# Performance work log

Hardware: AMD Instinct MI355X
Metric: run time of the kernel (lower is better)

Reference implementation:

```python
import jax, jax.numpy as jnp
import numpy as np

B, N, C, IC = 8, 4096, 1024, 256
EPS = 1e-5


def setup_inputs() -> dict:
    key = jax.random.key(0)
    ks = jax.random.split(key, 10)
    s = 0.02  # keep activations well-scaled
    return {
        "v": jax.random.normal(ks[0], (B, N, C), jnp.float32),
        "g_w": jax.random.normal(ks[1], (IC, C), jnp.float32) * s,
        "g_b": jax.random.normal(ks[2], (IC,), jnp.float32) * s,
        "theta_w": jax.random.normal(ks[3], (IC, C), jnp.float32) * s,
        "theta_b": jax.random.normal(ks[4], (IC,), jnp.float32) * s,
        "phi_w": jax.random.normal(ks[5], (IC, C), jnp.float32) * s,
        "phi_b": jax.random.normal(ks[6], (IC,), jnp.float32) * s,
        "W_w": jax.random.normal(ks[7], (C, IC), jnp.float32) * s,
        "W_b": jax.random.normal(ks[8], (C,), jnp.float32) * s,
        "bn_gamma": jnp.ones((C,), jnp.float32),
        "bn_beta": jnp.zeros((C,), jnp.float32),
    }


def reference(v, g_w, g_b, theta_w, theta_b, phi_w, phi_b, W_w, W_b, bn_gamma, bn_beta):
    # v: (B, N, C). All Conv1d(k=1) == per-token matmul.
    g_v = jnp.einsum("bnc,ic->bni", v, g_w) + g_b          # (B, N, IC)
    theta_v = jnp.einsum("bnc,ic->bni", v, theta_w) + theta_b
    phi_v = jnp.einsum("bnc,ic->bni", v, phi_w) + phi_b
    n = v.shape[1]
    # Affinity: R = theta @ phi^T, normalized by N (no softmax)
    R = jnp.einsum("bni,bmi->bnm", theta_v, phi_v) / n      # (B, N, N)
    y = jnp.einsum("bnm,bmi->bni", R, g_v)                  # (B, N, IC)
    W_y = jnp.einsum("bni,ci->bnc", y, W_w) + W_b           # (B, N, C)
    # BatchNorm1d training mode: per-channel stats over (B, N), biased var
    mean = jnp.mean(W_y, axis=(0, 1))
    var = jnp.var(W_y, axis=(0, 1))
    W_y = (W_y - mean) * jax.lax.rsqrt(var + EPS) * bn_gamma + bn_beta
    return W_y + v                                          # residual, (B, N, C)
```

## Files before the change

kernel.cpp:

```cpp
#include <hip/hip_runtime.h>
#include <hip/hip_bf16.h>
#include <stdint.h>


using bf16 = __hip_bfloat16;
typedef __attribute__((ext_vector_type(8))) short short8;
typedef __attribute__((ext_vector_type(4))) float f32x4;
typedef __attribute__((ext_vector_type(4))) short short4v;

#define DEVI static __device__ __forceinline__

DEVI float bf2f(unsigned short u) {
  union { unsigned int i; float f; } x; x.i = ((unsigned int)u) << 16; return x.f;
}
DEVI unsigned short f2bf(float f) {
  __hip_bfloat16 h = __float2bfloat16(f);
  return *reinterpret_cast<unsigned short*>(&h);
}

DEVI void gld16(const void* g, void* l) {
  __builtin_amdgcn_global_load_lds((__attribute__((address_space(1))) void*)g,
                                   (__attribute__((address_space(3))) void*)l,
                                   16, 0, 0);
}

DEVI short8 cvt8(float4 a, float4 b) {
  short8 o;
  o[0] = (short)f2bf(a.x); o[1] = (short)f2bf(a.y);
  o[2] = (short)f2bf(a.z); o[3] = (short)f2bf(a.w);
  o[4] = (short)f2bf(b.x); o[5] = (short)f2bf(b.y);
  o[6] = (short)f2bf(b.z); o[7] = (short)f2bf(b.w);
  return o;
}

DEVI void mfma_loop(const bf16* A, int ldA, const bf16* B, int ldB,
                    int kiters, bf16* lds_a, bf16* lds_b, f32x4 acc[4][4])
{
  const int tid = threadIdx.x;
  const int lane = tid & 63;
  const int w = tid >> 6;
  const int wr = w >> 1, wc = w & 1;
  const int srow = w * 32 + (lane >> 2);
  const int scol = (((lane & 3) ^ ((srow >> 1) & 3))) * 8;
  const bf16* ga0 = A + (size_t)srow * ldA + scol;
  const bf16* ga1 = A + (size_t)(srow + 16) * ldA + scol;
  const bf16* gb0 = B + (size_t)srow * ldB + scol;
  const bf16* gb1 = B + (size_t)(srow + 16) * ldB + scol;
  bf16* la0 = lds_a + w * 1024 + lane * 8;
  bf16* la1 = la0 + 512;
  bf16* lb0 = lds_b + w * 1024 + lane * 8;
  bf16* lb1 = lb0 + 512;
  const int frow = lane & 15;
  const int fk = (((lane >> 4) ^ ((frow >> 1) & 3))) * 8;
  const bf16* ra = lds_a + (wr * 64 + frow) * 32 + fk;
  const bf16* rb = lds_b + (wc * 64 + frow) * 32 + fk;
  for (int it = 0; it < kiters; ++it) {
    gld16(ga0, la0); gld16(ga1, la1);
    gld16(gb0, lb0); gld16(gb1, lb1);
    ga0 += 32; ga1 += 32; gb0 += 32; gb1 += 32;
    __syncthreads();
    short8 af[4], bfr[4];
#pragma unroll
    for (int i = 0; i < 4; ++i) af[i] = *(const short8*)(ra + i * 512);
#pragma unroll
    for (int j = 0; j < 4; ++j) bfr[j] = *(const short8*)(rb + j * 512);
#pragma unroll
    for (int i = 0; i < 4; ++i)
#pragma unroll
      for (int j = 0; j < 4; ++j)
        acc[i][j] = __builtin_amdgcn_mfma_f32_16x16x32_bf16(af[i], bfr[j], acc[i][j], 0, 0, 0);
    __syncthreads();
  }
}

DEVI void mfma_loop64(const bf16* A, int ldA, const bf16* B, int ldB,
                      int kiters64, bf16* lds_a, bf16* lds_b, f32x4 acc[4][4])
{
  const int tid = threadIdx.x;
  const int lane = tid & 63;
  const int w = tid >> 6;
  const int wr = w >> 1, wc = w & 1;
  const bf16* gA[4]; const bf16* gB[4]; bf16* dA[4]; bf16* dB[4];
#pragma unroll
  for (int s = 0; s < 4; ++s) {
    const int p = s * 256 + tid;
    const int ksub = p >> 9;
    const int row = (p >> 2) & 127;
    const int c2 = p & 3;
    gA[s] = A + (size_t)row * ldA + ksub * 32 + c2 * 8;
    gB[s] = B + (size_t)row * ldB + ksub * 32 + c2 * 8;
    dA[s] = lds_a + s * 2048 + w * 512 + lane * 8;
    dB[s] = lds_b + s * 2048 + w * 512 + lane * 8;
  }
  const int frow = lane & 15;
  const int fk = (lane >> 4) * 8;
  const bf16* ra = lds_a + (wr * 64 + frow) * 32 + fk;
  const bf16* rb = lds_b + (wc * 64 + frow) * 32 + fk;
  for (int it = 0; it < kiters64; ++it) {
#pragma unroll
    for (int s = 0; s < 4; ++s) gld16(gA[s], dA[s]);
#pragma unroll
    for (int s = 0; s < 4; ++s) gld16(gB[s], dB[s]);
#pragma unroll
    for (int s = 0; s < 4; ++s) { gA[s] += 64; gB[s] += 64; }
    __syncthreads();
#pragma unroll
    for (int kk = 0; kk < 2; ++kk) {
      short8 af[4], bfr[4];
#pragma unroll
      for (int i = 0; i < 4; ++i) af[i] = *(const short8*)(ra + kk * 4096 + i * 512);
#pragma unroll
      for (int j = 0; j < 4; ++j) bfr[j] = *(const short8*)(rb + kk * 4096 + j * 512);
#pragma unroll
      for (int i = 0; i < 4; ++i)
#pragma unroll
        for (int j = 0; j < 4; ++j)
          acc[i][j] = __builtin_amdgcn_mfma_f32_16x16x32_bf16(af[i], bfr[j], acc[i][j], 0, 0, 0);
    }
    __syncthreads();
  }
}

#define ACC_INIT(acc)                                   \
  _Pragma("unroll") for (int i = 0; i < 4; ++i)         \
  _Pragma("unroll") for (int j = 0; j < 4; ++j)         \
      acc[i][j] = (f32x4){0.f, 0.f, 0.f, 0.f};

__global__ __launch_bounds__(256) void k_cast_all(
    const float* __restrict__ v, bf16* __restrict__ vbf,
    const float* __restrict__ s0, const float* __restrict__ s1,
    const float* __restrict__ s2, const float* __restrict__ s3,
    bf16* __restrict__ d0, bf16* __restrict__ d1,
    bf16* __restrict__ d2, bf16* __restrict__ d3,
    float* __restrict__ zbuf)
{
  const int bx = blockIdx.x;
  if (bx == 16384 + 512) {
    float4 z = {0.f, 0.f, 0.f, 0.f};
    *(float4*)(zbuf + threadIdx.x * 8) = z;
    *(float4*)(zbuf + threadIdx.x * 8 + 4) = z;
    return;
  }
  const float* in; bf16* out; size_t base;
  if (bx < 16384) {
    in = v; out = vbf; base = (size_t)bx * 2048;
  } else {
    const int wq = bx - 16384;
    switch (wq >> 7) {
      case 0:  in = s0; out = d0; break;
      case 1:  in = s1; out = d1; break;
      case 2:  in = s2; out = d2; break;
      default: in = s3; out = d3; break;
    }
    base = (size_t)(wq & 127) * 2048;
  }
  const size_t idx = base + (size_t)threadIdx.x * 8;
  float4 a = *(const float4*)(in + idx);
  float4 b = *(const float4*)(in + idx + 4);
  *(short8*)(out + idx) = cvt8(a, b);
}

__global__ __launch_bounds__(256) void k_proj(
    const bf16* __restrict__ vbf,
    const bf16* __restrict__ w_th, const float* __restrict__ b_th,
    const bf16* __restrict__ w_ph, const float* __restrict__ b_ph,
    const bf16* __restrict__ w_g,  const float* __restrict__ b_g,
    bf16* __restrict__ theta, bf16* __restrict__ phiT, bf16* __restrict__ gT)
{
  __shared__ __align__(16) char smem[34048];
  bf16* lds_a = (bf16*)smem;
  bf16* lds_b = (bf16*)(smem + 16384);
  unsigned short* lds_t = (unsigned short*)smem;

  const int tt = blockIdx.x;
  const int yy = blockIdx.y;
  const int proj = yy >> 1;
  const int icb = (yy & 1) * 128;
  const bf16* wsel = (proj == 0) ? w_th : ((proj == 1) ? w_ph : w_g);
  const float* bsel = (proj == 0) ? b_th : ((proj == 1) ? b_ph : b_g);

  const size_t t0 = (size_t)tt * 128;
  f32x4 acc[4][4];
  ACC_INIT(acc);
  mfma_loop64(vbf + t0 * 1024, 1024, wsel + (size_t)icb * 1024, 1024, 16, lds_a, lds_b, acc);

  const int tid = threadIdx.x, lane = tid & 63, w = tid >> 6;
  const int wr = w >> 1, wc = w & 1, quad = lane >> 4, l15 = lane & 15;
  float biasv[4];
#pragma unroll
  for (int j = 0; j < 4; ++j) biasv[j] = bsel[icb + wc * 64 + j * 16 + l15];

  if (proj == 0) {
#pragma unroll
    for (int i = 0; i < 4; ++i)
#pragma unroll
      for (int j = 0; j < 4; ++j)
#pragma unroll
        for (int r = 0; r < 4; ++r) {
          int m = wr * 64 + i * 16 + quad * 4 + r;
          int n = wc * 64 + j * 16 + l15;
          theta[(t0 + m) * 256 + icb + n] = __float2bfloat16(acc[i][j][r] + biasv[j]);
        }
  } else {
#pragma unroll
    for (int i = 0; i < 4; ++i)
#pragma unroll
      for (int j = 0; j < 4; ++j)
#pragma unroll
        for (int r = 0; r < 4; ++r) {
          int m = wr * 64 + i * 16 + quad * 4 + r;
          int n = wc * 64 + j * 16 + l15;
          lds_t[m * 133 + n] = f2bf(acc[i][j][r] + biasv[j]);
        }
    __syncthreads();
    bf16* outT = (proj == 1) ? phiT : gT;
    const int bb = (int)(t0 >> 12);
    const int n0 = (int)(t0 & 4095);
    const int tg = tid & 7;
    const int ch0 = tid >> 3;
#pragma unroll
    for (int half = 0; half < 2; ++half)
#pragma unroll
      for (int cc = 0; cc < 4; ++cc) {
        int ch = ch0 + cc * 32;
        int tok0 = half * 64 + tg * 8;
        short8 pk;
#pragma unroll
        for (int r = 0; r < 8; ++r) pk[r] = (short)lds_t[(tok0 + r) * 133 + ch];
        *(short8*)(outT + ((size_t)(bb * 256 + icb + ch)) * 4096 + n0 + tok0) = pk;
      }
  }
}

__global__ __launch_bounds__(256) void k_affin(
    const bf16* __restrict__ phiT, const bf16* __restrict__ gT, float* __restrict__ Mp)
{
  __shared__ __align__(16) char smem[16384];
  bf16* lds_a = (bf16*)smem;
  bf16* lds_b = (bf16*)(smem + 8192);
  const int kc = blockIdx.x;
  const int jt = blockIdx.y >> 1;
  const int it2 = blockIdx.y & 1;
  const int bb = blockIdx.z;
  f32x4 acc[4][4];
  ACC_INIT(acc);
  const bf16* A = phiT + ((size_t)bb * 256 + jt * 128) * 4096 + kc * 512;
  const bf16* B = gT   + ((size_t)bb * 256 + it2 * 128) * 4096 + kc * 512;
  mfma_loop(A, 4096, B, 4096, 16, lds_a, lds_b, acc);
  const int tid = threadIdx.x, lane = tid & 63, w = tid >> 6;
  const int wr = w >> 1, wc = w & 1, quad = lane >> 4, l15 = lane & 15;
  float* Mb = Mp + ((size_t)kc * 8 + bb) * 65536;
#pragma unroll
  for (int i = 0; i < 4; ++i)
#pragma unroll
    for (int j = 0; j < 4; ++j)
#pragma unroll
      for (int r = 0; r < 4; ++r) {
        int m = wr * 64 + i * 16 + quad * 4 + r;
        int n = wc * 64 + j * 16 + l15;
        Mb[(size_t)(jt * 128 + m) * 256 + it2 * 128 + n] = acc[i][j][r];
      }
}

__global__ __launch_bounds__(256) void k_mconv(const float* __restrict__ Mp, bf16* __restrict__ Mbf)
{
  const size_t i = ((size_t)blockIdx.x * 256 + threadIdx.x) * 4;
  float4 s = *(const float4*)(Mp + i);
#pragma unroll
  for (int kc = 1; kc < 8; ++kc) {
    float4 p = *(const float4*)(Mp + (size_t)kc * 524288 + i);
    s.x += p.x; s.y += p.y; s.z += p.z; s.w += p.w;
  }
  short4v o;
  o[0] = (short)f2bf(s.x * (1.0f / 4096.0f));
  o[1] = (short)f2bf(s.y * (1.0f / 4096.0f));
  o[2] = (short)f2bf(s.z * (1.0f / 4096.0f));
  o[3] = (short)f2bf(s.w * (1.0f / 4096.0f));
  *(short4v*)(Mbf + i) = o;
}

__global__ __launch_bounds__(256) void k_pt(
    const bf16* __restrict__ Ww, const bf16* __restrict__ Mbf, bf16* __restrict__ PT)
{
  __shared__ __align__(16) char smem[16384];
  bf16* lds_a = (bf16*)smem;
  bf16* lds_b = (bf16*)(smem + 8192);
  const int ct = blockIdx.x;
  const int jt = blockIdx.y;
  const int bb = blockIdx.z;
  f32x4 acc[4][4];
  ACC_INIT(acc);
  mfma_loop(Ww + (size_t)ct * 128 * 256, 256,
            Mbf + ((size_t)bb * 256 + jt * 128) * 256, 256, 8, lds_a, lds_b, acc);
  const int tid = threadIdx.x, lane = tid & 63, w = tid >> 6;
  const int wr = w >> 1, wc = w & 1, quad = lane >> 4, l15 = lane & 15;
#pragma unroll
  for (int i = 0; i < 4; ++i)
#pragma unroll
    for (int j = 0; j < 4; ++j)
#pragma unroll
      for (int r = 0; r < 4; ++r) {
        int m = wr * 64 + i * 16 + quad * 4 + r;
        int n = wc * 64 + j * 16 + l15;
        PT[((size_t)bb * 1024 + ct * 128 + m) * 256 + jt * 128 + n] = __float2bfloat16(acc[i][j][r]);
      }
}

__global__ __launch_bounds__(256) void k_wy(
    const bf16* __restrict__ theta, const bf16* __restrict__ PT, bf16* __restrict__ Wy,
    float* __restrict__ sums, float* __restrict__ sumsq)
{
  __shared__ __align__(16) char smem[16384];
  bf16* lds_a = (bf16*)smem;
  bf16* lds_b = (bf16*)(smem + 8192);
  const size_t t0 = (size_t)blockIdx.x * 128;
  const int ct = blockIdx.y;
  const int bb = (int)(t0 >> 12);
  f32x4 acc[4][4];
  ACC_INIT(acc);
  mfma_loop(theta + t0 * 256, 256,
            PT + ((size_t)bb * 1024 + ct * 128) * 256, 256, 8, lds_a, lds_b, acc);
  const int tid = threadIdx.x, lane = tid & 63, w = tid >> 6;
  const int wr = w >> 1, wc = w & 1, quad = lane >> 4, l15 = lane & 15;
  float ps[4] = {0.f, 0.f, 0.f, 0.f}, pq[4] = {0.f, 0.f, 0.f, 0.f};
#pragma unroll
  for (int i = 0; i < 4; ++i)
#pragma unroll
    for (int j = 0; j < 4; ++j)
#pragma unroll
      for (int r = 0; r < 4; ++r) {
        int m = wr * 64 + i * 16 + quad * 4 + r;
        int n = wc * 64 + j * 16 + l15;
        float f = acc[i][j][r];
        Wy[(t0 + m) * 1024 + ct * 128 + n] = __float2bfloat16(f);
        ps[j] += f; pq[j] += f * f;
      }
#pragma unroll
  for (int j = 0; j < 4; ++j) {
    ps[j] += __shfl_xor(ps[j], 16); ps[j] += __shfl_xor(ps[j], 32);
    pq[j] += __shfl_xor(pq[j], 16); pq[j] += __shfl_xor(pq[j], 32);
  }
  if (quad == 0) {
#pragma unroll
    for (int j = 0; j < 4; ++j) {
      int c = ct * 128 + wc * 64 + j * 16 + l15;
      atomicAdd(&sums[c], ps[j]);
      atomicAdd(&sumsq[c], pq[j]);
    }
  }
}

__global__ __launch_bounds__(256) void k_out(const bf16* __restrict__ Wy, const float* __restrict__ v,
                                             const float* __restrict__ sums, const float* __restrict__ sumsq,
                                             const float* __restrict__ gamma, const float* __restrict__ beta,
                                             float* __restrict__ out)
{
  const size_t idx = ((size_t)blockIdx.x * 256 + threadIdx.x) * 4;
  const int c = (int)(idx & 1023);
  float4 sm = *(const float4*)(sums + c);
  float4 sq = *(const float4*)(sumsq + c);
  float4 gm = *(const float4*)(gamma + c);
  float4 bt = *(const float4*)(beta + c);
  short4v wv = *(const short4v*)(Wy + idx);
  float4 vv = *(const float4*)(v + idx);
  float4 o;
#pragma unroll
  for (int k = 0; k < 4; ++k) {
    float smk = (&sm.x)[k], sqk = (&sq.x)[k], gmk = (&gm.x)[k], btk = (&bt.x)[k];
    float mean = smk * (1.0f / 32768.0f);
    float var = sqk * (1.0f / 32768.0f) - mean * mean;
    float sc = gmk * rsqrtf(var + 1e-5f);
    float sh = btk - mean * sc;
    (&o.x)[k] = bf2f((unsigned short)wv[k]) * sc + sh + (&vv.x)[k];
  }
  *(float4*)(out + idx) = o;
}

extern "C" void kernel_launch(void* const* d_in, const int* in_sizes, int n_in,
                              void* d_out, int out_size, void* d_ws, size_t ws_size,
                              hipStream_t stream)
{
  (void)in_sizes; (void)n_in; (void)out_size; (void)ws_size;
  const float* v    = (const float*)d_in[0];
  const float* g_w  = (const float*)d_in[1];
  const float* g_b  = (const float*)d_in[2];
  const float* th_w = (const float*)d_in[3];
  const float* th_b = (const float*)d_in[4];
  const float* ph_w = (const float*)d_in[5];
  const float* ph_b = (const float*)d_in[6];
  const float* W_w  = (const float*)d_in[7];
  const float* gamma = (const float*)d_in[9];
  const float* beta  = (const float*)d_in[10];
  float* out = (float*)d_out;

  char* ws = (char*)d_ws;
  bf16* vbf  = (bf16*)ws;
  bf16* Wy   = (bf16*)ws;
  float* Mp  = (float*)ws;
  ws += (size_t)32768 * 1024 * 2;
  bf16* theta = (bf16*)ws;  ws += (size_t)32768 * 256 * 2;
  bf16* phiT  = (bf16*)ws;  ws += (size_t)32768 * 256 * 2;
  bf16* gT    = (bf16*)ws;  ws += (size_t)32768 * 256 * 2;
  bf16* Mbf   = (bf16*)ws;  ws += (size_t)8 * 65536 * 2;
  bf16* PT    = (bf16*)ws;  ws += (size_t)8 * 1024 * 256 * 2;
  bf16* thwb  = (bf16*)ws;  ws += (size_t)256 * 1024 * 2;
  bf16* phwb  = (bf16*)ws;  ws += (size_t)256 * 1024 * 2;
  bf16* gwb   = (bf16*)ws;  ws += (size_t)256 * 1024 * 2;
  bf16* Wwb   = (bf16*)ws;  ws += (size_t)1024 * 256 * 2;
  float* sums = (float*)ws; ws += 4096;
  float* sumsq= (float*)ws; ws += 4096;

  k_cast_all<<<16384 + 512 + 1, 256, 0, stream>>>(v, vbf, th_w, ph_w, g_w, W_w,
                                                  thwb, phwb, gwb, Wwb, sums);

  k_proj <<<dim3(256, 6), 256, 0, stream>>>(vbf, thwb, th_b, phwb, ph_b, gwb, g_b, theta, phiT, gT);
  k_affin<<<dim3(8, 4, 8), 256, 0, stream>>>(phiT, gT, Mp);
  k_mconv<<<512, 256, 0, stream>>>(Mp, Mbf);
  k_pt   <<<dim3(8, 2, 8), 256, 0, stream>>>(Wwb, Mbf, PT);
  k_wy   <<<dim3(256, 8), 256, 0, stream>>>(theta, PT, Wy, sums, sumsq);
  k_out  <<<32768, 256, 0, stream>>>(Wy, v, sums, sumsq, gamma, beta, out);
}
```

Before: 451.0 us.

## Enlarge projection GEMM tile to 256x128 with 512-thread blocks

The projection kernel now processes 256 tokens per block using 8 waves instead of 128 tokens with 4 waves. The shared weight (B) tile is loaded once per block for twice as many rows, which halves weight traffic per token. The transposed epilogue is split into two halves that reuse the LDS staging buffer. LDS use rises to 48KB per block and there are half as many blocks, which may lower occupancy and reduce latency hiding.

```diff
diff --git a/kernel.cpp b/kernel.cpp
--- a/kernel.cpp
+++ b/kernel.cpp
@@ -73,24 +73,32 @@
   }
 }
 
-DEVI void mfma_loop64(const bf16* A, int ldA, const bf16* B, int ldB,
-                      int kiters64, bf16* lds_a, bf16* lds_b, f32x4 acc[4][4])
+DEVI void mfma_loop_256x128(const bf16* A, int ldA, const bf16* B, int ldB,
+                            int kiters64, bf16* lds_a, bf16* lds_b, f32x4 acc[4][4])
 {
   const int tid = threadIdx.x;
   const int lane = tid & 63;
   const int w = tid >> 6;
   const int wr = w >> 1, wc = w & 1;
-  const bf16* gA[4]; const bf16* gB[4]; bf16* dA[4]; bf16* dB[4];
+  const bf16* gA[4]; bf16* dA[4];
 #pragma unroll
   for (int s = 0; s < 4; ++s) {
-    const int p = s * 256 + tid;
+    const int p = s * 512 + tid;
+    const int ksub = p >> 10;
+    const int row = (p >> 2) & 255;
+    const int c2 = p & 3;
+    gA[s] = A + (size_t)row * ldA + ksub * 32 + c2 * 8;
+    dA[s] = lds_a + p * 8;
+  }
+  const bf16* gB[2]; bf16* dB[2];
+#pragma unroll
+  for (int s = 0; s < 2; ++s) {
+    const int p = s * 512 + tid;
     const int ksub = p >> 9;
     const int row = (p >> 2) & 127;
     const int c2 = p & 3;
-    gA[s] = A + (size_t)row * ldA + ksub * 32 + c2 * 8;
     gB[s] = B + (size_t)row * ldB + ksub * 32 + c2 * 8;
-    dA[s] = lds_a + s * 2048 + w * 512 + lane * 8;
-    dB[s] = lds_b + s * 2048 + w * 512 + lane * 8;
+    dB[s] = lds_b + p * 8;
   }
   const int frow = lane & 15;
   const int fk = (lane >> 4) * 8;
@@ -100,15 +108,17 @@
 #pragma unroll
     for (int s = 0; s < 4; ++s) gld16(gA[s], dA[s]);
 #pragma unroll
-    for (int s = 0; s < 4; ++s) gld16(gB[s], dB[s]);
-#pragma unroll
-    for (int s = 0; s < 4; ++s) { gA[s] += 64; gB[s] += 64; }
+    for (int s = 0; s < 2; ++s) gld16(gB[s], dB[s]);
+#pragma unroll
+    for (int s = 0; s < 4; ++s) gA[s] += 64;
+#pragma unroll
+    for (int s = 0; s < 2; ++s) gB[s] += 64;
     __syncthreads();
 #pragma unroll
     for (int kk = 0; kk < 2; ++kk) {
       short8 af[4], bfr[4];
 #pragma unroll
-      for (int i = 0; i < 4; ++i) af[i] = *(const short8*)(ra + kk * 4096 + i * 512);
+      for (int i = 0; i < 4; ++i) af[i] = *(const short8*)(ra + kk * 8192 + i * 512);
 #pragma unroll
       for (int j = 0; j < 4; ++j) bfr[j] = *(const short8*)(rb + kk * 4096 + j * 512);
 #pragma unroll
@@ -160,16 +170,16 @@
   *(short8*)(out + idx) = cvt8(a, b);
 }
 
-__global__ __launch_bounds__(256) void k_proj(
+__global__ __launch_bounds__(512) void k_proj(
     const bf16* __restrict__ vbf,
     const bf16* __restrict__ w_th, const float* __restrict__ b_th,
     const bf16* __restrict__ w_ph, const float* __restrict__ b_ph,
     const bf16* __restrict__ w_g,  const float* __restrict__ b_g,
     bf16* __restrict__ theta, bf16* __restrict__ phiT, bf16* __restrict__ gT)
 {
-  __shared__ __align__(16) char smem[34048];
+  __shared__ __align__(16) char smem[49152];
   bf16* lds_a = (bf16*)smem;
-  bf16* lds_b = (bf16*)(smem + 16384);
+  bf16* lds_b = (bf16*)(smem + 32768);
   unsigned short* lds_t = (unsigned short*)smem;
 
   const int tt = blockIdx.x;
@@ -179,10 +189,11 @@
   const bf16* wsel = (proj == 0) ? w_th : ((proj == 1) ? w_ph : w_g);
   const float* bsel = (proj == 0) ? b_th : ((proj == 1) ? b_ph : b_g);
 
-  const size_t t0 = (size_t)tt * 128;
+  const size_t t0 = (size_t)tt * 256;
   f32x4 acc[4][4];
   ACC_INIT(acc);
-  mfma_loop64(vbf + t0 * 1024, 1024, wsel + (size_t)icb * 1024, 1024, 16, lds_a, lds_b, acc);
+  mfma_loop_256x128(vbf + t0 * 1024, 1024, wsel + (size_t)icb * 1024, 1024, 16,
+                    lds_a, lds_b, acc);
 
   const int tid = threadIdx.x, lane = tid & 63, w = tid >> 6;
   const int wr = w >> 1, wc = w & 1, quad = lane >> 4, l15 = lane & 15;
@@ -202,33 +213,36 @@
           theta[(t0 + m) * 256 + icb + n] = __float2bfloat16(acc[i][j][r] + biasv[j]);
         }
   } else {
-#pragma unroll
-    for (int i = 0; i < 4; ++i)
-#pragma unroll
-      for (int j = 0; j < 4; ++j)
-#pragma unroll
-        for (int r = 0; r < 4; ++r) {
-          int m = wr * 64 + i * 16 + quad * 4 + r;
-          int n = wc * 64 + j * 16 + l15;
-          lds_t[m * 133 + n] = f2bf(acc[i][j][r] + biasv[j]);
-        }
-    __syncthreads();
     bf16* outT = (proj == 1) ? phiT : gT;
     const int bb = (int)(t0 >> 12);
     const int n0 = (int)(t0 & 4095);
-    const int tg = tid & 7;
-    const int ch0 = tid >> 3;
-#pragma unroll
-    for (int half = 0; half < 2; ++half)
+    const int tg = tid & 15;
+    const int ch0 = tid >> 4;
+#pragma unroll
+    for (int h = 0; h < 2; ++h) {
+      __syncthreads();
+      if ((wr >> 1) == h) {
+#pragma unroll
+        for (int i = 0; i < 4; ++i)
+#pragma unroll
+          for (int j = 0; j < 4; ++j)
+#pragma unroll
+            for (int r = 0; r < 4; ++r) {
+              int mrow = (wr & 1) * 64 + i * 16 + quad * 4 + r;
+              int n = wc * 64 + j * 16 + l15;
+              lds_t[mrow * 133 + n] = f2bf(acc[i][j][r] + biasv[j]);
+            }
+      }
+      __syncthreads();
 #pragma unroll
       for (int cc = 0; cc < 4; ++cc) {
         int ch = ch0 + cc * 32;
-        int tok0 = half * 64 + tg * 8;
         short8 pk;
 #pragma unroll
-        for (int r = 0; r < 8; ++r) pk[r] = (short)lds_t[(tok0 + r) * 133 + ch];
-        *(short8*)(outT + ((size_t)(bb * 256 + icb + ch)) * 4096 + n0 + tok0) = pk;
+        for (int r = 0; r < 8; ++r) pk[r] = (short)lds_t[(tg * 8 + r) * 133 + ch];
+        *(short8*)(outT + ((size_t)(bb * 256 + icb + ch)) * 4096 + n0 + h * 128 + tg * 8) = pk;
       }
+    }
   }
 }
 
@@ -413,7 +427,7 @@
   k_cast_all<<<16384 + 512 + 1, 256, 0, stream>>>(v, vbf, th_w, ph_w, g_w, W_w,
                                                   thwb, phwb, gwb, Wwb, sums);
 
-  k_proj <<<dim3(256, 6), 256, 0, stream>>>(vbf, thwb, th_b, phwb, ph_b, gwb, g_b, theta, phiT, gT);
+  k_proj <<<dim3(128, 6), 512, 0, stream>>>(vbf, thwb, th_b, phwb, ph_b, gwb, g_b, theta, phiT, gT);
   k_affin<<<dim3(8, 4, 8), 256, 0, stream>>>(phiT, gT, Mp);
   k_mconv<<<512, 256, 0, stream>>>(Mp, Mbf);
   k_pt   <<<dim3(8, 2, 8), 256, 0, stream>>>(Wwb, Mbf, PT);
```

New measurement: 439.2 us. 2.6% less time.
